# Performance work log

Hardware: AMD Instinct MI355X
Metric: run time of the kernel (lower is better)

## Reference

```python
import jax, jax.numpy as jnp
import numpy as np

B, IN, H = 16384, 1024, 1024


def setup_inputs() -> dict:
    key = jax.random.key(0)
    ks = jax.random.split(key, 11)
    s = 1.0 / np.sqrt(IN + H)  # torch Linear init scale
    def lin(kw, kb):
        W = jax.random.uniform(kw, (H, IN + H), jnp.float32, -s, s)
        b = jax.random.uniform(kb, (H,), jnp.float32, -s, s)
        return W, b
    Wf, bf = lin(ks[0], ks[1])
    Wi, bi = lin(ks[2], ks[3])
    Wg, bg = lin(ks[4], ks[5])
    Wo, bo = lin(ks[6], ks[7])
    x = jax.random.normal(ks[8], (B, IN), jnp.float32)
    h_prev = jax.random.normal(ks[9], (B, H), jnp.float32)
    c_prev = jax.random.normal(ks[10], (B, H), jnp.float32)
    return {"x": x, "h_prev": h_prev, "c_prev": c_prev,
            "Wf": Wf, "bf": bf, "Wi": Wi, "bi": bi,
            "Wg": Wg, "bg": bg, "Wo": Wo, "bo": bo}


def reference(x, h_prev, c_prev, Wf, bf, Wi, bi, Wg, bg, Wo, bo):
    # combined: (B, IN+H)
    combined = jnp.concatenate([x, h_prev], axis=1)
    f_t = jax.nn.sigmoid(combined @ Wf.T + bf)
    i_t = jax.nn.sigmoid(combined @ Wi.T + bi)
    g_t = jnp.tanh(combined @ Wg.T + bg)
    o_t = jax.nn.sigmoid(combined @ Wo.T + bo)
    c_next = f_t * c_prev + i_t * g_t
    h_next = o_t * jnp.tanh(c_next)
    return (h_next, c_next)
```

## Files before the change

kernel.cpp:

```cpp
#include <hip/hip_runtime.h>
#include <stdint.h>


#define BB 16384
#define KK 2048
#define HH 1024
#define NN 4096

typedef float  f32x4  __attribute__((ext_vector_type(4)));
typedef __bf16 bf16x8 __attribute__((ext_vector_type(8)));
typedef short  s16x8  __attribute__((ext_vector_type(8)));

__device__ __forceinline__ ushort f2bf(float f) {
  uint32_t x = __float_as_uint(f);
  x += 0x7fffu + ((x >> 16) & 1u);
  return (ushort)(x >> 16);
}
__device__ __forceinline__ float bf2f(ushort h) {
  return __uint_as_float(((uint32_t)h) << 16);
}

__device__ __forceinline__ void split8(const float* __restrict__ src, s16x8* hi, s16x8* lo) {
  float4 v0 = *(const float4*)src;
  float4 v1 = *(const float4*)(src + 4);
  float f[8] = {v0.x, v0.y, v0.z, v0.w, v1.x, v1.y, v1.z, v1.w};
  s16x8 h, l;
#pragma unroll
  for (int j = 0; j < 8; ++j) {
    ushort hb = f2bf(f[j]);
    float  r  = f[j] - bf2f(hb);
    h[j] = (short)hb;
    l[j] = (short)f2bf(r);
  }
  *hi = h; *lo = l;
}

__global__ void prep_A(const float* __restrict__ x, const float* __restrict__ hp,
                       ushort* __restrict__ Ahi, ushort* __restrict__ Alo) {
  size_t i8 = ((size_t)blockIdx.x * 256 + threadIdx.x) * 8;
  int b = (int)(i8 >> 11);
  int k = (int)(i8 & 2047);
  const float* src = (k < 1024) ? (x + (size_t)b * 1024 + k)
                                : (hp + (size_t)b * 1024 + (k - 1024));
  s16x8 h, l;
  split8(src, &h, &l);
  int swz = (b >> 1) & 3;
  size_t dst = (size_t)b * KK + (size_t)(k ^ (swz << 3));
  *(s16x8*)(Ahi + dst) = h;
  *(s16x8*)(Alo + dst) = l;
}

__global__ void prep_W(const float* __restrict__ Wf, const float* __restrict__ Wi,
                       const float* __restrict__ Wg, const float* __restrict__ Wo,
                       const float* __restrict__ bf_, const float* __restrict__ bi_,
                       const float* __restrict__ bg_, const float* __restrict__ bo_,
                       ushort* __restrict__ Whi, ushort* __restrict__ Wlo,
                       float* __restrict__ bpack) {
  size_t i8 = ((size_t)blockIdx.x * 256 + threadIdx.x) * 8;
  int n = (int)(i8 >> 11);
  int k = (int)(i8 & 2047);
  int g = n & 3, h = n >> 2;
  const float* w = (g == 0) ? Wf : (g == 1) ? Wi : (g == 2) ? Wg : Wo;
  s16x8 hi, lo;
  split8(w + (size_t)h * KK + k, &hi, &lo);
  int swz = (n >> 1) & 3;
  size_t dst = (size_t)n * KK + (size_t)(k ^ (swz << 3));
  *(s16x8*)(Whi + dst) = hi;
  *(s16x8*)(Wlo + dst) = lo;
  if (k == 0) {
    const float* bb = (g == 0) ? bf_ : (g == 1) ? bi_ : (g == 2) ? bg_ : bo_;
    bpack[n] = bb[h];
  }
}

__device__ __forceinline__ void gl2lds16(const ushort* g, ushort* l) {
  auto gp = reinterpret_cast<const __attribute__((address_space(1))) uint32_t*>(
      reinterpret_cast<uintptr_t>(g));
  auto lp = reinterpret_cast<__attribute__((address_space(3))) uint32_t*>(
      reinterpret_cast<uintptr_t>(l));
  __builtin_amdgcn_global_load_lds(gp, lp, 16, 0, 0);
}

__global__ __launch_bounds__(256) void lstm_gemm(
    const ushort* __restrict__ Ahi, const ushort* __restrict__ Alo,
    const ushort* __restrict__ Whi, const ushort* __restrict__ Wlo,
    const float* __restrict__ bpack, const float* __restrict__ c_prev,
    float* __restrict__ out) {
  __shared__ ushort lds[4][128 * 32];

  int t = threadIdx.x;
  int lane = t & 63;
  int wave = t >> 6;
  int wm = wave >> 1, wn = wave & 1;
  int mbase = blockIdx.y * 128;
  int nbase = blockIdx.x * 128;

  f32x4 acc[4][4];
#pragma unroll
  for (int mi = 0; mi < 4; ++mi)
#pragma unroll
    for (int ni = 0; ni < 4; ++ni) acc[mi][ni] = f32x4{0.f, 0.f, 0.f, 0.f};

  int lr = lane & 15;
  int uo = ((lane >> 4) ^ ((lane >> 1) & 3)) * 8;
  int srow = t >> 2;
  int su = t & 3;
  int ldsw = (t & ~63) * 8;

  for (int kt = 0; kt < KK / 32; ++kt) {
    int ko = kt * 32;
#pragma unroll
    for (int c = 0; c < 2; ++c) {
      int row = c * 64 + srow;
      size_t aoff = (size_t)(mbase + row) * KK + ko + su * 8;
      size_t boff = (size_t)(nbase + row) * KK + ko + su * 8;
      int lo_ = c * 2048 + ldsw;
      gl2lds16(Ahi + aoff, &lds[0][lo_]);
      gl2lds16(Alo + aoff, &lds[1][lo_]);
      gl2lds16(Whi + boff, &lds[2][lo_]);
      gl2lds16(Wlo + boff, &lds[3][lo_]);
    }
    __syncthreads();

    s16x8 ah[4], al[4], bh[4], bl[4];
#pragma unroll
    for (int mi = 0; mi < 4; ++mi) {
      int off = (wm * 64 + mi * 16 + lr) * 32 + uo;
      ah[mi] = *(const s16x8*)&lds[0][off];
      al[mi] = *(const s16x8*)&lds[1][off];
    }
#pragma unroll
    for (int ni = 0; ni < 4; ++ni) {
      int off = (wn * 64 + ni * 16 + lr) * 32 + uo;
      bh[ni] = *(const s16x8*)&lds[2][off];
      bl[ni] = *(const s16x8*)&lds[3][off];
    }
#pragma unroll
    for (int mi = 0; mi < 4; ++mi)
#pragma unroll
      for (int ni = 0; ni < 4; ++ni) {
        bf16x8 a_h = __builtin_bit_cast(bf16x8, ah[mi]);
        bf16x8 a_l = __builtin_bit_cast(bf16x8, al[mi]);
        bf16x8 b_h = __builtin_bit_cast(bf16x8, bh[ni]);
        bf16x8 b_l = __builtin_bit_cast(bf16x8, bl[ni]);
        acc[mi][ni] = __builtin_amdgcn_mfma_f32_16x16x32_bf16(a_h, b_h, acc[mi][ni], 0, 0, 0);
        acc[mi][ni] = __builtin_amdgcn_mfma_f32_16x16x32_bf16(a_h, b_l, acc[mi][ni], 0, 0, 0);
        acc[mi][ni] = __builtin_amdgcn_mfma_f32_16x16x32_bf16(a_l, b_h, acc[mi][ni], 0, 0, 0);
      }
    __syncthreads();
  }

  int g = lr & 3;
#pragma unroll
  for (int mi = 0; mi < 4; ++mi)
#pragma unroll
    for (int ni = 0; ni < 4; ++ni) {
      int n_g = nbase + wn * 64 + ni * 16 + lr;
      float bias = bpack[n_g];
      int h = n_g >> 2;
      int m0 = mbase + wm * 64 + mi * 16 + (lane >> 4) * 4;
#pragma unroll
      for (int r = 0; r < 4; ++r) {
        float v = acc[mi][ni][r] + bias;
        float t1 = __shfl_xor(v, 1, 64);
        float t2 = __shfl_xor(v, 2, 64);
        float t3 = __shfl_xor(v, 3, 64);
        float fv = (g == 0) ? v : (g == 1) ? t1 : (g == 2) ? t2 : t3;
        float iv = (g == 1) ? v : (g == 0) ? t1 : (g == 3) ? t2 : t3;
        float gv = (g == 2) ? v : (g == 3) ? t1 : (g == 0) ? t2 : t3;
        float ov = (g == 3) ? v : (g == 2) ? t1 : (g == 1) ? t2 : t3;
        int m = m0 + r;
        float cp = c_prev[(size_t)m * HH + h];
        float ft = 1.f / (1.f + __expf(-fv));
        float it = 1.f / (1.f + __expf(-iv));
        float gt = tanhf(gv);
        float ot = 1.f / (1.f + __expf(-ov));
        float cn = ft * cp + it * gt;
        float hn = ot * tanhf(cn);
        if (g == 0)      out[(size_t)m * HH + h] = hn;
        else if (g == 1) out[(size_t)BB * HH + (size_t)m * HH + h] = cn;
      }
    }
}

__global__ void lstm_naive(const float* __restrict__ x, const float* __restrict__ hp,
                           const float* __restrict__ cp,
                           const float* __restrict__ Wf, const float* __restrict__ bf_,
                           const float* __restrict__ Wi, const float* __restrict__ bi_,
                           const float* __restrict__ Wg, const float* __restrict__ bg_,
                           const float* __restrict__ Wo, const float* __restrict__ bo_,
                           float* __restrict__ out) {
  size_t idx = (size_t)blockIdx.x * 256 + threadIdx.x;
  int b = (int)(idx >> 10), h = (int)(idx & 1023);
  float sf = bf_[h], si = bi_[h], sg = bg_[h], so = bo_[h];
  const float* xr = x + (size_t)b * 1024;
  const float* hr = hp + (size_t)b * 1024;
  const float* wf = Wf + (size_t)h * KK;
  const float* wi = Wi + (size_t)h * KK;
  const float* wg = Wg + (size_t)h * KK;
  const float* wo = Wo + (size_t)h * KK;
  for (int k = 0; k < 1024; ++k) {
    float a = xr[k];
    sf += a * wf[k]; si += a * wi[k]; sg += a * wg[k]; so += a * wo[k];
  }
  for (int k = 0; k < 1024; ++k) {
    float a = hr[k];
    sf += a * wf[1024 + k]; si += a * wi[1024 + k];
    sg += a * wg[1024 + k]; so += a * wo[1024 + k];
  }
  float ft = 1.f / (1.f + expf(-sf));
  float it = 1.f / (1.f + expf(-si));
  float gt = tanhf(sg);
  float ot = 1.f / (1.f + expf(-so));
  float cn = ft * cp[idx] + it * gt;
  out[idx] = ot * tanhf(cn);
  out[(size_t)BB * HH + idx] = cn;
}

extern "C" void kernel_launch(void* const* d_in, const int* in_sizes, int n_in,
                              void* d_out, int out_size, void* d_ws, size_t ws_size,
                              hipStream_t stream) {
  const float* x  = (const float*)d_in[0];
  const float* hp = (const float*)d_in[1];
  const float* cp = (const float*)d_in[2];
  const float* Wf = (const float*)d_in[3];  const float* bf_ = (const float*)d_in[4];
  const float* Wi = (const float*)d_in[5];  const float* bi_ = (const float*)d_in[6];
  const float* Wg = (const float*)d_in[7];  const float* bg_ = (const float*)d_in[8];
  const float* Wo = (const float*)d_in[9];  const float* bo_ = (const float*)d_in[10];
  float* out = (float*)d_out;

  const size_t offAhi = 0;
  const size_t offAlo = (size_t)BB * KK * 2;
  const size_t offWhi = offAlo + (size_t)BB * KK * 2;
  const size_t offWlo = offWhi + (size_t)NN * KK * 2;
  const size_t offBp  = offWlo + (size_t)NN * KK * 2;
  const size_t needed = offBp + (size_t)NN * 4;

  if (ws_size < needed) {
    lstm_naive<<<(BB * HH) / 256, 256, 0, stream>>>(x, hp, cp, Wf, bf_, Wi, bi_, Wg, bg_, Wo, bo_, out);
    return;
  }

  ushort* Ahi = (ushort*)((char*)d_ws + offAhi);
  ushort* Alo = (ushort*)((char*)d_ws + offAlo);
  ushort* WhiP = (ushort*)((char*)d_ws + offWhi);
  ushort* WloP = (ushort*)((char*)d_ws + offWlo);
  float*  bpack = (float*)((char*)d_ws + offBp);

  prep_A<<<(BB * KK / 8) / 256, 256, 0, stream>>>(x, hp, Ahi, Alo);
  prep_W<<<(NN * KK / 8) / 256, 256, 0, stream>>>(Wf, Wi, Wg, Wo, bf_, bi_, bg_, bo_, WhiP, WloP, bpack);
  lstm_gemm<<<dim3(NN / 128, BB / 128), 256, 0, stream>>>(Ahi, Alo, WhiP, WloP, bpack, cp, out);
}
```

Baseline: 1.385 ms.

## Restructure split-bf16 GEMM into 256x256 tiles with 4-stage LDS pipeline

```diff
diff --git a/kernel.cpp b/kernel.cpp
--- a/kernel.cpp
+++ b/kernel.cpp
@@ -6,6 +6,7 @@
 #define KK 2048
 #define HH 1024
 #define NN 4096
+#define KSTEPS 192
 
 typedef float  f32x4  __attribute__((ext_vector_type(4)));
 typedef __bf16 bf16x8 __attribute__((ext_vector_type(8)));
@@ -81,84 +82,117 @@
   __builtin_amdgcn_global_load_lds(gp, lp, 16, 0, 0);
 }
 
-__global__ __launch_bounds__(256) void lstm_gemm(
+#define LSTM_STEP(S_, STAGE_EN_)                                               \
+  {                                                                            \
+    const int cur_ = (S_) & 3;                                                 \
+    const ushort* lA_ = &lds[cur_][0][0];                                      \
+    const ushort* lB_ = &lds[cur_][1][0];                                      \
+    s16x8 af_[4], bfv_[4];                                                     \
+    _Pragma("unroll") for (int mi = 0; mi < 4; ++mi)                           \
+        af_[mi] = *(const s16x8*)(lA_ + aoffL[mi]);                            \
+    _Pragma("unroll") for (int ni = 0; ni < 4; ++ni)                           \
+        bfv_[ni] = *(const s16x8*)(lB_ + boffL[ni]);                           \
+    if (STAGE_EN_) STAGE_A((S_) + 3, ((S_) + 3) & 3);                          \
+    __builtin_amdgcn_s_barrier();                                              \
+    __builtin_amdgcn_s_setprio(1);                                             \
+    _Pragma("unroll") for (int mi = 0; mi < 4; ++mi)                           \
+      _Pragma("unroll") for (int ni = 0; ni < 4; ++ni)                         \
+          acc[mi][ni] = __builtin_amdgcn_mfma_f32_16x16x32_bf16(               \
+              __builtin_bit_cast(bf16x8, af_[mi]),                             \
+              __builtin_bit_cast(bf16x8, bfv_[ni]), acc[mi][ni], 0, 0, 0);     \
+    __builtin_amdgcn_s_setprio(0);                                             \
+    __builtin_amdgcn_s_barrier();                                              \
+    _Pragma("unroll") for (int mi = 0; mi < 4; ++mi)                           \
+        af_[mi] = *(const s16x8*)(lA_ + aoffL[4 + mi]);                        \
+    if (STAGE_EN_) STAGE_B((S_) + 3, ((S_) + 3) & 3);                          \
+    __builtin_amdgcn_s_barrier();                                              \
+    __builtin_amdgcn_s_setprio(1);                                             \
+    _Pragma("unroll") for (int mi = 0; mi < 4; ++mi)                           \
+      _Pragma("unroll") for (int ni = 0; ni < 4; ++ni)                         \
+          acc[4 + mi][ni] = __builtin_amdgcn_mfma_f32_16x16x32_bf16(           \
+              __builtin_bit_cast(bf16x8, af_[mi]),                             \
+              __builtin_bit_cast(bf16x8, bfv_[ni]), acc[4 + mi][ni], 0, 0, 0); \
+    __builtin_amdgcn_s_setprio(0);                                             \
+  }
+
+__global__ __launch_bounds__(512, 2) void lstm_gemm8(
     const ushort* __restrict__ Ahi, const ushort* __restrict__ Alo,
     const ushort* __restrict__ Whi, const ushort* __restrict__ Wlo,
     const float* __restrict__ bpack, const float* __restrict__ c_prev,
     float* __restrict__ out) {
-  __shared__ ushort lds[4][128 * 32];
-
-  int t = threadIdx.x;
-  int lane = t & 63;
-  int wave = t >> 6;
-  int wm = wave >> 1, wn = wave & 1;
-  int mbase = blockIdx.y * 128;
-  int nbase = blockIdx.x * 128;
-
-  f32x4 acc[4][4];
-#pragma unroll
-  for (int mi = 0; mi < 4; ++mi)
+  __shared__ ushort lds[4][2][8192];
+
+  const int t = threadIdx.x;
+  const int lane = t & 63;
+  const int wave = t >> 6;
+  const int wm = wave >> 2;
+  const int wn = wave & 3;
+  const int mbase = blockIdx.y * 256;
+  const int nbase = blockIdx.x * 256;
+
+  const int lr = lane & 15;
+  const int uo = ((lane >> 4) ^ ((lane >> 1) & 3)) * 8;
+
+  int aoffL[8], boffL[4];
+#pragma unroll
+  for (int mi = 0; mi < 8; ++mi) aoffL[mi] = (wm * 128 + mi * 16 + lr) * 32 + uo;
+#pragma unroll
+  for (int ni = 0; ni < 4; ++ni) boffL[ni] = (wn * 64 + ni * 16 + lr) * 32 + uo;
+
+  const size_t arow = (size_t)(mbase + (t >> 2)) * KK + (size_t)(t & 3) * 8;
+  const size_t brow = (size_t)(nbase + (t >> 2)) * KK + (size_t)(t & 3) * 8;
+  const int ldsStageOff = (t & ~63) * 8;
+
+  auto STAGE_A = [&](int sv, int r) {
+    int ksl = sv * 32;
+    int seg = ksl >> 11;
+    int kcol = ksl & 2047;
+    const ushort* ap = (seg == 1) ? Alo : Ahi;
+    gl2lds16(ap + arow + kcol,            &lds[r][0][ldsStageOff]);
+    gl2lds16(ap + arow + 128 * KK + kcol, &lds[r][0][4096 + ldsStageOff]);
+  };
+  auto STAGE_B = [&](int sv, int r) {
+    int ksl = sv * 32;
+    int seg = ksl >> 11;
+    int kcol = ksl & 2047;
+    const ushort* bp = (seg == 2) ? Wlo : Whi;
+    gl2lds16(bp + brow + kcol,            &lds[r][1][ldsStageOff]);
+    gl2lds16(bp + brow + 128 * KK + kcol, &lds[r][1][4096 + ldsStageOff]);
+  };
+
+  f32x4 acc[8][4];
+#pragma unroll
+  for (int mi = 0; mi < 8; ++mi)
 #pragma unroll
     for (int ni = 0; ni < 4; ++ni) acc[mi][ni] = f32x4{0.f, 0.f, 0.f, 0.f};
 
-  int lr = lane & 15;
-  int uo = ((lane >> 4) ^ ((lane >> 1) & 3)) * 8;
-  int srow = t >> 2;
-  int su = t & 3;
-  int ldsw = (t & ~63) * 8;
-
-  for (int kt = 0; kt < KK / 32; ++kt) {
-    int ko = kt * 32;
-#pragma unroll
-    for (int c = 0; c < 2; ++c) {
-      int row = c * 64 + srow;
-      size_t aoff = (size_t)(mbase + row) * KK + ko + su * 8;
-      size_t boff = (size_t)(nbase + row) * KK + ko + su * 8;
-      int lo_ = c * 2048 + ldsw;
-      gl2lds16(Ahi + aoff, &lds[0][lo_]);
-      gl2lds16(Alo + aoff, &lds[1][lo_]);
-      gl2lds16(Whi + boff, &lds[2][lo_]);
-      gl2lds16(Wlo + boff, &lds[3][lo_]);
-    }
-    __syncthreads();
-
-    s16x8 ah[4], al[4], bh[4], bl[4];
-#pragma unroll
-    for (int mi = 0; mi < 4; ++mi) {
-      int off = (wm * 64 + mi * 16 + lr) * 32 + uo;
-      ah[mi] = *(const s16x8*)&lds[0][off];
-      al[mi] = *(const s16x8*)&lds[1][off];
-    }
+  STAGE_A(0, 0); STAGE_B(0, 0);
+  STAGE_A(1, 1); STAGE_B(1, 1);
+  STAGE_A(2, 2); STAGE_B(2, 2);
+  asm volatile("s_waitcnt vmcnt(8)" ::: "memory");
+  __builtin_amdgcn_s_barrier();
+
+  for (int s = 0; s < KSTEPS - 3; ++s) {
+    LSTM_STEP(s, 1);
+    asm volatile("s_waitcnt vmcnt(8)" ::: "memory");
+    __builtin_amdgcn_s_barrier();
+  }
+  asm volatile("s_waitcnt vmcnt(0)" ::: "memory");
+  __builtin_amdgcn_s_barrier();
+  for (int s = KSTEPS - 3; s < KSTEPS; ++s) {
+    LSTM_STEP(s, 0);
+    __builtin_amdgcn_s_barrier();
+  }
+
+  const int g = lr & 3;
+#pragma unroll
+  for (int mi = 0; mi < 8; ++mi) {
+    const int m0 = mbase + wm * 128 + mi * 16 + (lane >> 4) * 4;
 #pragma unroll
     for (int ni = 0; ni < 4; ++ni) {
-      int off = (wn * 64 + ni * 16 + lr) * 32 + uo;
-      bh[ni] = *(const s16x8*)&lds[2][off];
-      bl[ni] = *(const s16x8*)&lds[3][off];
-    }
-#pragma unroll
-    for (int mi = 0; mi < 4; ++mi)
-#pragma unroll
-      for (int ni = 0; ni < 4; ++ni) {
-        bf16x8 a_h = __builtin_bit_cast(bf16x8, ah[mi]);
-        bf16x8 a_l = __builtin_bit_cast(bf16x8, al[mi]);
-        bf16x8 b_h = __builtin_bit_cast(bf16x8, bh[ni]);
-        bf16x8 b_l = __builtin_bit_cast(bf16x8, bl[ni]);
-        acc[mi][ni] = __builtin_amdgcn_mfma_f32_16x16x32_bf16(a_h, b_h, acc[mi][ni], 0, 0, 0);
-        acc[mi][ni] = __builtin_amdgcn_mfma_f32_16x16x32_bf16(a_h, b_l, acc[mi][ni], 0, 0, 0);
-        acc[mi][ni] = __builtin_amdgcn_mfma_f32_16x16x32_bf16(a_l, b_h, acc[mi][ni], 0, 0, 0);
-      }
-    __syncthreads();
-  }
-
-  int g = lr & 3;
-#pragma unroll
-  for (int mi = 0; mi < 4; ++mi)
-#pragma unroll
-    for (int ni = 0; ni < 4; ++ni) {
-      int n_g = nbase + wn * 64 + ni * 16 + lr;
-      float bias = bpack[n_g];
-      int h = n_g >> 2;
-      int m0 = mbase + wm * 64 + mi * 16 + (lane >> 4) * 4;
+      const int n_g = nbase + wn * 64 + ni * 16 + lr;
+      const float bias = bpack[n_g];
+      const int h = n_g >> 2;
 #pragma unroll
       for (int r = 0; r < 4; ++r) {
         float v = acc[mi][ni][r] + bias;
@@ -181,6 +215,7 @@
         else if (g == 1) out[(size_t)BB * HH + (size_t)m * HH + h] = cn;
       }
     }
+  }
 }
 
 __global__ void lstm_naive(const float* __restrict__ x, const float* __restrict__ hp,
@@ -249,5 +284,5 @@
 
   prep_A<<<(BB * KK / 8) / 256, 256, 0, stream>>>(x, hp, Ahi, Alo);
   prep_W<<<(NN * KK / 8) / 256, 256, 0, stream>>>(Wf, Wi, Wg, Wo, bf_, bi_, bg_, bo_, WhiP, WloP, bpack);
-  lstm_gemm<<<dim3(NN / 128, BB / 128), 256, 0, stream>>>(Ahi, Alo, WhiP, WloP, bpack, cp, out);
-}
+  lstm_gemm8<<<dim3(NN / 256, BB / 256), 512, 0, stream>>>(Ahi, Alo, WhiP, WloP, bpack, cp, out);
+}
```

Result: no change. 1.401 ms (+1.2%).
